# Kernel optimization log

Hardware: AMD Instinct MI355X
Metric: run time of the kernel (lower is better)

The kernel has to match this reference:

```python
import jax, jax.numpy as jnp
import numpy as np

N, D, NUM_CLASSES = 1024, 256, 10
EPS = 1e-12


def setup_inputs() -> dict:
    key = jax.random.key(0)
    k1, k2, k3, k4 = jax.random.split(key, 4)
    return {
        "fm_s": jax.random.normal(k1, (N, D), dtype=jnp.float32),
        "fm_t": jax.random.normal(k2, (N, D), dtype=jnp.float32),
        "logvar_s": jax.random.normal(k3, (N, D), dtype=jnp.float32),
        "targets": jax.random.randint(k4, (N,), 0, NUM_CLASSES, dtype=jnp.int64),
        "fusion_true": 0,  # False branch (no multi_index)
    }


def reference(fm_s, fm_t, logvar_s, targets, fusion_true):
    # pairwise squared diff scaled by per-row (student) variance: (N, N, D)
    diff2 = (fm_s[:, None, :] - fm_t[None, :, :]) ** 2
    inv_var_term = diff2 / (2.0 * jnp.exp(logvar_s)[:, None, :] + EPS)
    half_lv = 0.5 * logvar_s[:, None, :]
    lp = jax.nn.relu(inv_var_term + half_lv).sum(-1)   # (N, N)
    ln = jax.nn.relu(-inv_var_term - half_lv).sum(-1)  # (N, N)
    pos = (targets[:, None] == targets[None, :]).astype(fm_s.dtype)  # self_mask_pos
    neg = 1.0 - pos
    loss_pos = lp * pos / pos.sum(-1, keepdims=True)
    loss_neg = ln * neg / neg.sum(-1, keepdims=True)
    # fusion_true == False path
    return loss_pos.sum(-1).mean() + loss_neg.sum(-1).mean()
```

## Files before the change

### kernel.cpp

```cpp
#include <hip/hip_runtime.h>
#include <math.h>

#define NN   1024
#define DD   256
#define NCLS 10

#define TI 64
#define TJ 128
#define DC 32
#define DSPLIT 8
#define NBLK ((NN / TI) * (NN / TJ) * DSPLIT)

typedef float f32x2 __attribute__((ext_vector_type(2)));
typedef float f32x4 __attribute__((ext_vector_type(4)));

#define PK_FMA(d, a, b, c) \
    asm("v_pk_fma_f32 %0, %1, %2, %3" : "=v"(d) : "v"(a), "v"(b), "v"(c))
#define PK_ADD(d, a, b) \
    asm("v_pk_add_f32 %0, %1, %2" : "=v"(d) : "v"(a), "v"(b))
#define PK_ACC(acc, x) \
    asm("v_pk_add_f32 %0, %0, %1" : "+v"(acc) : "v"(x))

__global__ __launch_bounds__(256) void pair_kernel(
    const float* __restrict__ fm_s, const float* __restrict__ fm_t,
    const float* __restrict__ lv, const long long* __restrict__ tgt,
    float* __restrict__ partials)
{
    __shared__ float Al[TI * DC];
    __shared__ float Bl[TI * DC];
    __shared__ float Vl[TI * DC];
    __shared__ float Fl[TJ * DC];
    __shared__ int   ch[16];

    const int bid  = blockIdx.x;
    const int tile = bid >> 3;
    const int kd   = bid & 7;
    const int i0   = (tile >> 3) * TI;
    const int j0   = (tile & 7) * TJ;
    const int doff = kd * DC;

    const int tid  = threadIdx.x;
    const int tx   = tid & 15;
    const int ty   = tid >> 4;
    const int lane = tid & 63;
    const int w    = tid >> 6;

    const int* tgt32 = (const int*)tgt;

    if (tid < 16) ch[tid] = 0;

    const int srow = tid >> 3;
    const int sq   = tid & 7;
#pragma unroll
    for (int p = 0; p < 4; ++p) {
        const int r = p * 32 + srow;
        f32x4 v = *(const f32x4*)&fm_t[(j0 + r) * DD + doff + sq * 4];
        const int phys = (sq + (r >> 3)) & 7;
        *(f32x4*)&Fl[r * DC + phys * 4] = v;
    }
#pragma unroll
    for (int p = 0; p < 2; ++p) {
        const int r = p * 32 + srow;
        const int g = (i0 + r) * DD + doff + sq * 4;
        f32x4 fs = *(const f32x4*)&fm_s[g];
        f32x4 l  = *(const f32x4*)&lv[g];
        f32x4 A, B, V;
#pragma unroll
        for (int e = 0; e < 4; ++e) {
            const float iv = 0.5f * __expf(-l[e]);
            const float fsiv = fs[e] * iv;
            A[e] = fmaf(fsiv, fs[e], 0.5f * l[e]);
            B[e] = -2.0f * fsiv;
            V[e] = iv;
        }
        const int phys = (sq + (r >> 2)) & 7;
        *(f32x4*)&Al[r * DC + phys * 4] = A;
        *(f32x4*)&Bl[r * DC + phys * 4] = B;
        *(f32x4*)&Vl[r * DC + phys * 4] = V;
    }

    __syncthreads();
#pragma unroll
    for (int k = 0; k < 4; ++k)
        atomicAdd(&ch[tgt32[(k * 256 + tid) * 2]], 1);

    __syncthreads();

    f32x2 s1v[4][8];
    float s2[4][8];
#pragma unroll
    for (int a = 0; a < 4; ++a)
#pragma unroll
        for (int b = 0; b < 8; ++b) { s1v[a][b] = (f32x2)(0.f); s2[a][b] = 0.f; }

#pragma unroll
    for (int k = 0; k < 8; ++k) {
        const int iq = ((k + ty) & 7) * 4;
        const f32x4* pa = (const f32x4*)&Al[ty * 128 + iq];
        const f32x4* pb = (const f32x4*)&Bl[ty * 128 + iq];
        const f32x4* pv = (const f32x4*)&Vl[ty * 128 + iq];
        f32x4 fa[4], fb[4], fv[4];
#pragma unroll
        for (int r = 0; r < 4; ++r) {
            fa[r] = pa[r * 8];
            fb[r] = pb[r * 8];
            fv[r] = pv[r * 8];
        }
        const f32x4* pf = (const f32x4*)&Fl[tx * 256 + ((k + tx) & 7) * 4];
#pragma unroll
        for (int rj = 0; rj < 8; ++rj) {
            const f32x4 f = pf[rj * 8];
            const f32x2 f01 = f.lo, f23 = f.hi;
#pragma unroll
            for (int ri = 0; ri < 4; ++ri) {
                f32x2 u01, u23, t01, t23, st;
                PK_FMA(u01, fv[ri].lo, f01, fb[ri].lo);
                PK_FMA(u23, fv[ri].hi, f23, fb[ri].hi);
                PK_FMA(t01, u01, f01, fa[ri].lo);
                PK_FMA(t23, u23, f23, fa[ri].hi);
                PK_ADD(st, t01, t23);
                PK_ACC(s1v[ri][rj], st);
                s2[ri][rj] += (fabsf(t01.x) + fabsf(t01.y))
                            + (fabsf(t23.x) + fabsf(t23.y));
            }
        }
    }

    float csum = 0.f;
#pragma unroll
    for (int ri = 0; ri < 4; ++ri) {
        const int t   = tgt32[(i0 + ty * 4 + ri) * 2];
        const int cnt = ch[t];
        const float wp = 1.0f / (float)cnt;
        const float wn = 1.0f / (float)(NN - cnt);
#pragma unroll
        for (int rj = 0; rj < 8; ++rj) {
            const int tj = tgt32[(j0 + tx * 8 + rj) * 2];
            const float s1 = s1v[ri][rj].x + s1v[ri][rj].y;
            const float lp = 0.5f * (s2[ri][rj] + s1);
            const float ln = 0.5f * (s2[ri][rj] - s1);
            csum += (t == tj) ? lp * wp : ln * wn;
        }
    }

#pragma unroll
    for (int off = 32; off > 0; off >>= 1) csum += __shfl_down(csum, off);
    __syncthreads();
    if (lane == 0) Al[w] = csum;
    __syncthreads();
    if (tid == 0) partials[bid] = (Al[0] + Al[1]) + (Al[2] + Al[3]);
}

__global__ __launch_bounds__(256) void finalize_kernel(const float* __restrict__ partials,
                                                       float* __restrict__ out) {
    __shared__ float red[256];
    const int tid = threadIdx.x;
    red[tid] = (partials[tid] + partials[tid + 256]) +
               (partials[tid + 512] + partials[tid + 768]);
    __syncthreads();
    for (int s = 128; s > 0; s >>= 1) {
        if (tid < s) red[tid] += red[tid + s];
        __syncthreads();
    }
    if (tid == 0) out[0] = red[0] * (1.0f / (float)NN);
}

extern "C" void kernel_launch(void* const* d_in, const int* in_sizes, int n_in,
                              void* d_out, int out_size, void* d_ws, size_t ws_size,
                              hipStream_t stream) {
    const float* fm_s    = (const float*)d_in[0];
    const float* fm_t    = (const float*)d_in[1];
    const float* lv      = (const float*)d_in[2];
    const long long* tgt = (const long long*)d_in[3];

    float* partials = (float*)d_ws;

    hipLaunchKernelGGL(pair_kernel, dim3(NBLK), dim3(256), 0, stream,
                       fm_s, fm_t, lv, tgt, partials);
    hipLaunchKernelGGL(finalize_kernel, dim3(1), dim3(256), 0, stream,
                       partials, (float*)d_out);
}
```

Baseline: 39.34 us.

## Precompute class weights in separate kernel and reorder inner loop for F reuse

Moves the per-class count histogram out of every pair block into a tiny count_kernel that writes reciprocal weights to workspace, removing a shared-memory atomic pass and one barrier per block. The inner loop is reordered so the eight F vectors are loaded once per k-step and the A/B/V rows are streamed, and the packed s1 accumulator becomes two scalar adds. In exchange it adds an extra kernel launch, extra global reads of the weight table, and possibly more scalar ALU work from unpacking s1.

```diff
diff --git a/kernel.cpp b/kernel.cpp
--- a/kernel.cpp
+++ b/kernel.cpp
@@ -18,19 +18,30 @@
     asm("v_pk_fma_f32 %0, %1, %2, %3" : "=v"(d) : "v"(a), "v"(b), "v"(c))
 #define PK_ADD(d, a, b) \
     asm("v_pk_add_f32 %0, %1, %2" : "=v"(d) : "v"(a), "v"(b))
-#define PK_ACC(acc, x) \
-    asm("v_pk_add_f32 %0, %0, %1" : "+v"(acc) : "v"(x))
+
+__global__ __launch_bounds__(256) void count_kernel(const long long* __restrict__ tgt,
+                                                    float* __restrict__ wtab) {
+    __shared__ int c[NCLS];
+    int tid = threadIdx.x;
+    if (tid < NCLS) c[tid] = 0;
+    __syncthreads();
+    for (int k = tid; k < NN; k += 256) atomicAdd(&c[(int)tgt[k]], 1);
+    __syncthreads();
+    if (tid < NCLS) {
+        wtab[tid]      = 1.0f / (float)c[tid];
+        wtab[16 + tid] = 1.0f / (float)(NN - c[tid]);
+    }
+}
 
 __global__ __launch_bounds__(256) void pair_kernel(
     const float* __restrict__ fm_s, const float* __restrict__ fm_t,
     const float* __restrict__ lv, const long long* __restrict__ tgt,
-    float* __restrict__ partials)
+    const float* __restrict__ wtab, float* __restrict__ partials)
 {
     __shared__ float Al[TI * DC];
     __shared__ float Bl[TI * DC];
     __shared__ float Vl[TI * DC];
     __shared__ float Fl[TJ * DC];
-    __shared__ int   ch[16];
 
     const int bid  = blockIdx.x;
     const int tile = bid >> 3;
@@ -46,8 +57,6 @@
     const int w    = tid >> 6;
 
     const int* tgt32 = (const int*)tgt;
-
-    if (tid < 16) ch[tid] = 0;
 
     const int srow = tid >> 3;
     const int sq   = tid & 7;
@@ -80,46 +89,39 @@
     }
 
     __syncthreads();
-#pragma unroll
-    for (int k = 0; k < 4; ++k)
-        atomicAdd(&ch[tgt32[(k * 256 + tid) * 2]], 1);
 
-    __syncthreads();
-
-    f32x2 s1v[4][8];
-    float s2[4][8];
+    float s1[4][8], s2[4][8];
 #pragma unroll
     for (int a = 0; a < 4; ++a)
 #pragma unroll
-        for (int b = 0; b < 8; ++b) { s1v[a][b] = (f32x2)(0.f); s2[a][b] = 0.f; }
+        for (int b = 0; b < 8; ++b) { s1[a][b] = 0.f; s2[a][b] = 0.f; }
 
 #pragma unroll
     for (int k = 0; k < 8; ++k) {
+        const f32x4* pf = (const f32x4*)&Fl[tx * 256 + ((k + tx) & 7) * 4];
+        f32x4 f[8];
+#pragma unroll
+        for (int rj = 0; rj < 8; ++rj) f[rj] = pf[rj * 8];
+
         const int iq = ((k + ty) & 7) * 4;
         const f32x4* pa = (const f32x4*)&Al[ty * 128 + iq];
         const f32x4* pb = (const f32x4*)&Bl[ty * 128 + iq];
         const f32x4* pv = (const f32x4*)&Vl[ty * 128 + iq];
-        f32x4 fa[4], fb[4], fv[4];
 #pragma unroll
-        for (int r = 0; r < 4; ++r) {
-            fa[r] = pa[r * 8];
-            fb[r] = pb[r * 8];
-            fv[r] = pv[r * 8];
-        }
-        const f32x4* pf = (const f32x4*)&Fl[tx * 256 + ((k + tx) & 7) * 4];
+        for (int ri = 0; ri < 4; ++ri) {
+            const f32x4 fa = pa[ri * 8];
+            const f32x4 fb = pb[ri * 8];
+            const f32x4 fv = pv[ri * 8];
 #pragma unroll
-        for (int rj = 0; rj < 8; ++rj) {
-            const f32x4 f = pf[rj * 8];
-            const f32x2 f01 = f.lo, f23 = f.hi;
-#pragma unroll
-            for (int ri = 0; ri < 4; ++ri) {
+            for (int rj = 0; rj < 8; ++rj) {
+                const f32x2 f01 = f[rj].lo, f23 = f[rj].hi;
                 f32x2 u01, u23, t01, t23, st;
-                PK_FMA(u01, fv[ri].lo, f01, fb[ri].lo);
-                PK_FMA(u23, fv[ri].hi, f23, fb[ri].hi);
-                PK_FMA(t01, u01, f01, fa[ri].lo);
-                PK_FMA(t23, u23, f23, fa[ri].hi);
+                PK_FMA(u01, fv.lo, f01, fb.lo);
+                PK_FMA(u23, fv.hi, f23, fb.hi);
+                PK_FMA(t01, u01, f01, fa.lo);
+                PK_FMA(t23, u23, f23, fa.hi);
                 PK_ADD(st, t01, t23);
-                PK_ACC(s1v[ri][rj], st);
+                s1[ri][rj] += st.x + st.y;
                 s2[ri][rj] += (fabsf(t01.x) + fabsf(t01.y))
                             + (fabsf(t23.x) + fabsf(t23.y));
             }
@@ -130,15 +132,13 @@
 #pragma unroll
     for (int ri = 0; ri < 4; ++ri) {
         const int t   = tgt32[(i0 + ty * 4 + ri) * 2];
-        const int cnt = ch[t];
-        const float wp = 1.0f / (float)cnt;
-        const float wn = 1.0f / (float)(NN - cnt);
+        const float wp = wtab[t];
+        const float wn = wtab[16 + t];
 #pragma unroll
         for (int rj = 0; rj < 8; ++rj) {
             const int tj = tgt32[(j0 + tx * 8 + rj) * 2];
-            const float s1 = s1v[ri][rj].x + s1v[ri][rj].y;
-            const float lp = 0.5f * (s2[ri][rj] + s1);
-            const float ln = 0.5f * (s2[ri][rj] - s1);
+            const float lp = 0.5f * (s2[ri][rj] + s1[ri][rj]);
+            const float ln = 0.5f * (s2[ri][rj] - s1[ri][rj]);
             csum += (t == tj) ? lp * wp : ln * wn;
         }
     }
@@ -173,10 +173,12 @@
     const float* lv      = (const float*)d_in[2];
     const long long* tgt = (const long long*)d_in[3];
 
-    float* partials = (float*)d_ws;
+    float* wtab     = (float*)d_ws;
+    float* partials = (float*)((char*)d_ws + 256);
 
+    hipLaunchKernelGGL(count_kernel, dim3(1), dim3(256), 0, stream, tgt, wtab);
     hipLaunchKernelGGL(pair_kernel, dim3(NBLK), dim3(256), 0, stream,
-                       fm_s, fm_t, lv, tgt, partials);
+                       fm_s, fm_t, lv, tgt, wtab, partials);
     hipLaunchKernelGGL(finalize_kernel, dim3(1), dim3(256), 0, stream,
                        partials, (float*)d_out);
 }
```

New measurement: 37.82 us. 1.04x faster.
